# Performance work log

Measured on AMD Instinct MI355X. Metric: run time of the kernel, lower is better.

Reference implementation:

```python
import jax, jax.numpy as jnp
import numpy as np

K1, K2 = 3, 3
DIL = 1
PAD = (DIL * (K1 - 1) // 2, DIL * (K2 - 1) // 2)


def _unfold(x, k1, k2, dilation, padding):
    # x: [B, C, H, W] -> patches [B, C, k1*k2, H*W], matching F.unfold ordering
    B, C, H, W = x.shape
    p0, p1 = padding
    xp = jnp.pad(x, ((0, 0), (0, 0), (p0, p0), (p1, p1)))
    cols = []
    for i in range(k1):  # small fixed loop over kernel taps
        for j in range(k2):
            cols.append(xp[:, :, i * dilation:i * dilation + H, j * dilation:j * dilation + W])
    patches = jnp.stack(cols, axis=2)  # [B, C, k1*k2, H, W]
    return patches.reshape(B, C, k1 * k2, H * W)


def setup_inputs() -> dict:
    key = jax.random.key(0)
    k1, k2, k3, k4 = jax.random.split(key, 4)
    B, Cin, Cout, H, W = 32, 128, 128, 32, 32
    x = jax.random.normal(k1, (B, Cin, H, W), dtype=jnp.float32)
    mask = jax.random.uniform(k2, (1, K1 * K2, H * W), dtype=jnp.float32)
    weight = jax.random.normal(k3, (Cout, Cin, K1, K2), dtype=jnp.float32) * 0.05
    bias = jax.random.normal(k4, (Cout,), dtype=jnp.float32) * 0.05
    return {"x": x, "mask": mask, "weight": weight, "bias": bias}


def reference(x, mask, weight, bias):
    B, Cin, H, W = x.shape
    Cout = weight.shape[0]
    KK = K1 * K2
    # unfold -> [B, Cin, KK, L]
    patches = _unfold(x, K1, K2, DIL, PAD)
    # per-patch mask multiply (mask broadcasts over B and Cin): mask [1, KK, L]
    patches = patches * mask[:, None, :, :]  # [B, Cin, KK, L]
    # dense matmul with flattened weight [Cout, Cin*KK]
    wm = weight.reshape(Cout, Cin * KK)
    out = jnp.einsum('ok,bkl->bol', wm, patches.reshape(B, Cin * KK, H * W))
    out = out + bias[None, :, None]
    return out.reshape(B, Cout, H, W)
```

## Files before the change

kernel.cpp:

```cpp
#include <hip/hip_runtime.h>
#include <hip/hip_fp16.h>

typedef _Float16 half8 __attribute__((ext_vector_type(8)));
typedef float f32x4 __attribute__((ext_vector_type(4)));

#define CIN   128
#define COUT  128
#define HH    32
#define WW    32
#define LTOT  1024
#define KKT   9
#define KDIM  1152

#define ABUF  32768
#define BOFF  65536
#define SMEM_BYTES 114688

__global__ void prep_w_kernel(const float* __restrict__ w, _Float16* __restrict__ wt) {
  int i = blockIdx.x * 256 + threadIdx.x;
  int o = i / KDIM;
  int r = i - o * KDIM;
  int kk = r >> 7, c = r & 127;
  wt[i] = (_Float16)w[(o * CIN + c) * KKT + kk];
}

__device__ __forceinline__ void gld16(const char* g, char* l) {
  __builtin_amdgcn_global_load_lds(
      (const __attribute__((address_space(1))) void*)g,
      (__attribute__((address_space(3))) void*)l, 16, 0, 0);
}

__global__ __launch_bounds__(512, 2)
void conv_mfma_kernel(const float* __restrict__ x,
                      const _Float16* __restrict__ wt,
                      const float* __restrict__ mask,
                      const float* __restrict__ bias,
                      float* __restrict__ out) {
  extern __shared__ char smem[];
  const int tid = threadIdx.x;
  int bid = blockIdx.x;
  bid = (bid & 7) * 32 + (bid >> 3);
  const int b  = bid >> 3;
  const int l0 = (bid & 7) << 7;
  const int h0 = (bid & 7) << 2;

  const int lane = tid & 63, wid = tid >> 6;
  const int lr = lane & 15, lg = lane >> 4;
  const int kh = wid >> 2;
  const int wq = wid & 3;
  const int mw = (wq >> 1) << 6;
  const int nw = (wq & 1) << 6;

  float mv[9][4];
  {
    const float* mr = mask + l0 + nw + lr;
#pragma unroll
    for (int kk = 0; kk < 9; ++kk)
#pragma unroll
      for (int nj = 0; nj < 4; ++nj)
        mv[kk][nj] = mr[kk * LTOT + nj * 16];
  }

  const int wv = tid & 31, q16 = tid >> 5;
  char* bdst = smem + BOFF + wv * 256 + ((q16 ^ (wv & 15)) << 4);
  const float* xb = x + (size_t)b * CIN * LTOT;
  {
    float fr[6][8];
#pragma unroll
    for (int r = 0; r < 6; ++r) {
      const int hg = h0 - 1 + r;
      if ((unsigned)hg < (unsigned)HH) {
        const float* s = xb + (size_t)q16 * 8 * LTOT + hg * WW + wv;
#pragma unroll
        for (int j = 0; j < 8; ++j) fr[r][j] = s[(size_t)j * LTOT];
      }
    }
    asm volatile("s_waitcnt vmcnt(0)" ::: "memory");
#pragma unroll
    for (int r = 0; r < 6; ++r) {
      const int hg = h0 - 1 + r;
      half8 v = (half8){0, 0, 0, 0, 0, 0, 0, 0};
      if ((unsigned)hg < (unsigned)HH) {
#pragma unroll
        for (int j = 0; j < 8; ++j) v[j] = (_Float16)fr[r][j];
      }
      *(half8*)(bdst + r * 8192) = v;
    }
  }
#pragma unroll
  for (int kk = 0; kk < 9; ++kk)
#pragma unroll
    for (int nj = 0; nj < 4; ++nj)
      asm volatile("" : "+v"(mv[kk][nj]));

  const int t4 = tid >> 4, ch = tid & 15;
  const int cx = (ch ^ (t4 & 15)) << 4;
  int asrc[4];
#pragma unroll
  for (int r = 0; r < 4; ++r) asrc[r] = (r * 32 + t4) * 2304 + cx;
  const char* wtc = (const char*)wt;
  auto stageA = [&](int kk) {
    const char* s = wtc + kk * 256;
    char* d = smem + (kk & 1) * ABUF + tid * 16;
#pragma unroll
    for (int r = 0; r < 4; ++r) gld16(s + asrc[r], d + r * 8192);
  };
  stageA(0);
  stageA(1);
  asm volatile("s_waitcnt lgkmcnt(0)" ::: "memory");

  f32x4 acc[4][4];
#pragma unroll
  for (int mi = 0; mi < 4; ++mi)
#pragma unroll
    for (int nj = 0; nj < 4; ++nj)
      acc[mi][nj] = (f32x4){0.f, 0.f, 0.f, 0.f};

#pragma unroll
  for (int kk = 0; kk < 9; ++kk) {
    if (kk < 8) asm volatile("s_waitcnt vmcnt(4)" ::: "memory");
    else        asm volatile("s_waitcnt vmcnt(0)" ::: "memory");
    __builtin_amdgcn_s_barrier();

    const char* A = smem + (kk & 1) * ABUF;
    const int di = (kk * 11) >> 5;
    const int dj = kk - 3 * di;

    const char* Bp[4];
    int xk[4];
    _Float16 mh[4];
#pragma unroll
    for (int nj = 0; nj < 4; ++nj) {
      const int wb = ((nj & 1) << 4) + lr + dj - 1;
      const bool vld = (unsigned)wb < (unsigned)WW;
      const int wc = vld ? wb : 0;
      const int hrow = (nw >> 5) + (nj >> 1) + di;
      Bp[nj] = smem + BOFF + hrow * 8192 + wc * 256;
      xk[nj] = wc & 15;
      mh[nj] = (_Float16)(vld ? mv[kk][nj] : 0.f);
    }
    const char* A0 = A + (mw + lr) * 256;

    __builtin_amdgcn_s_setprio(1);
#pragma unroll
    for (int s = 0; s < 2; ++s) {
      const int q = (kh * 2 + s) * 4 + lg;
      half8 a0 = *(const half8*)(A0 +     0 + ((q ^ lr) << 4));
      half8 a1 = *(const half8*)(A0 +  4096 + ((q ^ lr) << 4));
      half8 a2 = *(const half8*)(A0 +  8192 + ((q ^ lr) << 4));
      half8 a3 = *(const half8*)(A0 + 12288 + ((q ^ lr) << 4));
      half8 b0 = *(const half8*)(Bp[0] + ((q ^ xk[0]) << 4)) * mh[0];
      half8 b1 = *(const half8*)(Bp[1] + ((q ^ xk[1]) << 4)) * mh[1];
      half8 b2 = *(const half8*)(Bp[2] + ((q ^ xk[2]) << 4)) * mh[2];
      half8 b3 = *(const half8*)(Bp[3] + ((q ^ xk[3]) << 4)) * mh[3];
      acc[0][0] = __builtin_amdgcn_mfma_f32_16x16x32_f16(a0, b0, acc[0][0], 0, 0, 0);
      acc[1][0] = __builtin_amdgcn_mfma_f32_16x16x32_f16(a1, b0, acc[1][0], 0, 0, 0);
      acc[2][0] = __builtin_amdgcn_mfma_f32_16x16x32_f16(a2, b0, acc[2][0], 0, 0, 0);
      acc[3][0] = __builtin_amdgcn_mfma_f32_16x16x32_f16(a3, b0, acc[3][0], 0, 0, 0);
      acc[0][1] = __builtin_amdgcn_mfma_f32_16x16x32_f16(a0, b1, acc[0][1], 0, 0, 0);
      acc[1][1] = __builtin_amdgcn_mfma_f32_16x16x32_f16(a1, b1, acc[1][1], 0, 0, 0);
      acc[2][1] = __builtin_amdgcn_mfma_f32_16x16x32_f16(a2, b1, acc[2][1], 0, 0, 0);
      acc[3][1] = __builtin_amdgcn_mfma_f32_16x16x32_f16(a3, b1, acc[3][1], 0, 0, 0);
      acc[0][2] = __builtin_amdgcn_mfma_f32_16x16x32_f16(a0, b2, acc[0][2], 0, 0, 0);
      acc[1][2] = __builtin_amdgcn_mfma_f32_16x16x32_f16(a1, b2, acc[1][2], 0, 0, 0);
      acc[2][2] = __builtin_amdgcn_mfma_f32_16x16x32_f16(a2, b2, acc[2][2], 0, 0, 0);
      acc[3][2] = __builtin_amdgcn_mfma_f32_16x16x32_f16(a3, b2, acc[3][2], 0, 0, 0);
      acc[0][3] = __builtin_amdgcn_mfma_f32_16x16x32_f16(a0, b3, acc[0][3], 0, 0, 0);
      acc[1][3] = __builtin_amdgcn_mfma_f32_16x16x32_f16(a1, b3, acc[1][3], 0, 0, 0);
      acc[2][3] = __builtin_amdgcn_mfma_f32_16x16x32_f16(a2, b3, acc[2][3], 0, 0, 0);
      acc[3][3] = __builtin_amdgcn_mfma_f32_16x16x32_f16(a3, b3, acc[3][3], 0, 0, 0);
    }
    __builtin_amdgcn_s_setprio(0);

    asm volatile("s_waitcnt lgkmcnt(0)" ::: "memory");
    __builtin_amdgcn_s_barrier();
    if (kk <= 6) stageA(kk + 2);
  }

  char* red = smem + wq * 17408 + lane * 272;
  if (kh == 1) {
#pragma unroll
    for (int mi = 0; mi < 4; ++mi)
#pragma unroll
      for (int nj = 0; nj < 4; ++nj)
        *(f32x4*)(red + (mi * 4 + nj) * 16) = acc[mi][nj];
  }
  asm volatile("s_waitcnt lgkmcnt(0)" ::: "memory");
  __builtin_amdgcn_s_barrier();

  if (kh == 0) {
#pragma unroll
    for (int mi = 0; mi < 4; ++mi)
#pragma unroll
      for (int nj = 0; nj < 4; ++nj) {
        f32x4 p = *(const f32x4*)(red + (mi * 4 + nj) * 16);
        acc[mi][nj].x += p.x; acc[mi][nj].y += p.y;
        acc[mi][nj].z += p.z; acc[mi][nj].w += p.w;
      }

    float* outb = out + (size_t)b * COUT * LTOT + l0;
#pragma unroll
    for (int mi = 0; mi < 4; ++mi) {
#pragma unroll
      for (int rr = 0; rr < 4; ++rr) {
        const int o = mw + mi * 16 + lg * 4 + rr;
        const float bv = bias[o];
        float* orow = outb + (size_t)o * LTOT + nw + lr;
#pragma unroll
        for (int nj = 0; nj < 4; ++nj)
          orow[nj * 16] = acc[mi][nj][rr] + bv;
      }
    }
  }
}

extern "C" void kernel_launch(void* const* d_in, const int* in_sizes, int n_in,
                              void* d_out, int out_size, void* d_ws, size_t ws_size,
                              hipStream_t stream) {
  const float* x    = (const float*)d_in[0];
  const float* mask = (const float*)d_in[1];
  const float* w    = (const float*)d_in[2];
  const float* bias = (const float*)d_in[3];
  float* out = (float*)d_out;
  _Float16* wt = (_Float16*)d_ws;

  (void)hipFuncSetAttribute(reinterpret_cast<const void*>(conv_mfma_kernel),
                            hipFuncAttributeMaxDynamicSharedMemorySize, SMEM_BYTES);

  prep_w_kernel<<<576, 256, 0, stream>>>(w, wt);
  conv_mfma_kernel<<<256, 512, SMEM_BYTES, stream>>>(x, wt, mask, bias, out);
}
```

Before: 25.31 us.

## Read weight fragments directly from global memory in MFMA layout, drop LDS staging

The weight prep kernel now writes the fp16 weights pre-permuted into the exact per-lane MFMA fragment order. The conv kernel then loads A operands straight from global memory (L2-resident) instead of double-buffering them through LDS with async loads and per-tap barriers. This removes the per-iteration barriers and the LDS traffic for weights, and shrinks LDS use, which may allow more blocks per CU. In exchange, every wave issues its own global loads with latency exposed inside the MFMA loop, and weight reads are repeated across waves that share the same rows.

```diff
diff --git a/kernel.cpp b/kernel.cpp
--- a/kernel.cpp
+++ b/kernel.cpp
@@ -12,22 +12,16 @@
 #define KKT   9
 #define KDIM  1152
 
-#define ABUF  32768
-#define BOFF  65536
-#define SMEM_BYTES 114688
+#define SMEM_BYTES 69632
 
 __global__ void prep_w_kernel(const float* __restrict__ w, _Float16* __restrict__ wt) {
   int i = blockIdx.x * 256 + threadIdx.x;
-  int o = i / KDIM;
-  int r = i - o * KDIM;
-  int kk = r >> 7, c = r & 127;
+  int q = i >> 10;
+  int o = (i >> 3) & 127;
+  int j = i & 7;
+  int kk = q >> 4;
+  int c  = ((q & 15) << 3) + j;
   wt[i] = (_Float16)w[(o * CIN + c) * KKT + kk];
-}
-
-__device__ __forceinline__ void gld16(const char* g, char* l) {
-  __builtin_amdgcn_global_load_lds(
-      (const __attribute__((address_space(1))) void*)g,
-      (__attribute__((address_space(3))) void*)l, 16, 0, 0);
 }
 
 __global__ __launch_bounds__(512, 2)
@@ -62,7 +56,7 @@
   }
 
   const int wv = tid & 31, q16 = tid >> 5;
-  char* bdst = smem + BOFF + wv * 256 + ((q16 ^ (wv & 15)) << 4);
+  char* bdst = smem + wv * 256 + ((q16 ^ (wv & 15)) << 4);
   const float* xb = x + (size_t)b * CIN * LTOT;
   {
     float fr[6][8];
@@ -92,22 +86,9 @@
 #pragma unroll
     for (int nj = 0; nj < 4; ++nj)
       asm volatile("" : "+v"(mv[kk][nj]));
-
-  const int t4 = tid >> 4, ch = tid & 15;
-  const int cx = (ch ^ (t4 & 15)) << 4;
-  int asrc[4];
-#pragma unroll
-  for (int r = 0; r < 4; ++r) asrc[r] = (r * 32 + t4) * 2304 + cx;
-  const char* wtc = (const char*)wt;
-  auto stageA = [&](int kk) {
-    const char* s = wtc + kk * 256;
-    char* d = smem + (kk & 1) * ABUF + tid * 16;
-#pragma unroll
-    for (int r = 0; r < 4; ++r) gld16(s + asrc[r], d + r * 8192);
-  };
-  stageA(0);
-  stageA(1);
-  asm volatile("s_waitcnt lgkmcnt(0)" ::: "memory");
+  __syncthreads();
+
+  const char* abase = (const char*)wt + lg * 2048 + (mw + lr) * 16;
 
   f32x4 acc[4][4];
 #pragma unroll
@@ -118,11 +99,6 @@
 
 #pragma unroll
   for (int kk = 0; kk < 9; ++kk) {
-    if (kk < 8) asm volatile("s_waitcnt vmcnt(4)" ::: "memory");
-    else        asm volatile("s_waitcnt vmcnt(0)" ::: "memory");
-    __builtin_amdgcn_s_barrier();
-
-    const char* A = smem + (kk & 1) * ABUF;
     const int di = (kk * 11) >> 5;
     const int dj = kk - 3 * di;
 
@@ -135,24 +111,25 @@
       const bool vld = (unsigned)wb < (unsigned)WW;
       const int wc = vld ? wb : 0;
       const int hrow = (nw >> 5) + (nj >> 1) + di;
-      Bp[nj] = smem + BOFF + hrow * 8192 + wc * 256;
+      Bp[nj] = smem + hrow * 8192 + wc * 256;
       xk[nj] = wc & 15;
       mh[nj] = (_Float16)(vld ? mv[kk][nj] : 0.f);
     }
-    const char* A0 = A + (mw + lr) * 256;
 
     __builtin_amdgcn_s_setprio(1);
 #pragma unroll
     for (int s = 0; s < 2; ++s) {
-      const int q = (kh * 2 + s) * 4 + lg;
-      half8 a0 = *(const half8*)(A0 +     0 + ((q ^ lr) << 4));
-      half8 a1 = *(const half8*)(A0 +  4096 + ((q ^ lr) << 4));
-      half8 a2 = *(const half8*)(A0 +  8192 + ((q ^ lr) << 4));
-      half8 a3 = *(const half8*)(A0 + 12288 + ((q ^ lr) << 4));
-      half8 b0 = *(const half8*)(Bp[0] + ((q ^ xk[0]) << 4)) * mh[0];
-      half8 b1 = *(const half8*)(Bp[1] + ((q ^ xk[1]) << 4)) * mh[1];
-      half8 b2 = *(const half8*)(Bp[2] + ((q ^ xk[2]) << 4)) * mh[2];
-      half8 b3 = *(const half8*)(Bp[3] + ((q ^ xk[3]) << 4)) * mh[3];
+      const int qb = kk * 16 + (kh * 2 + s) * 4;
+      const char* ab = abase + qb * 2048;
+      const int q = qb + lg;
+      half8 a0 = *(const half8*)(ab);
+      half8 a1 = *(const half8*)(ab + 256);
+      half8 a2 = *(const half8*)(ab + 512);
+      half8 a3 = *(const half8*)(ab + 768);
+      half8 b0 = *(const half8*)(Bp[0] + (((q & 15) ^ xk[0]) << 4)) * mh[0];
+      half8 b1 = *(const half8*)(Bp[1] + (((q & 15) ^ xk[1]) << 4)) * mh[1];
+      half8 b2 = *(const half8*)(Bp[2] + (((q & 15) ^ xk[2]) << 4)) * mh[2];
+      half8 b3 = *(const half8*)(Bp[3] + (((q & 15) ^ xk[3]) << 4)) * mh[3];
       acc[0][0] = __builtin_amdgcn_mfma_f32_16x16x32_f16(a0, b0, acc[0][0], 0, 0, 0);
       acc[1][0] = __builtin_amdgcn_mfma_f32_16x16x32_f16(a1, b0, acc[1][0], 0, 0, 0);
       acc[2][0] = __builtin_amdgcn_mfma_f32_16x16x32_f16(a2, b0, acc[2][0], 0, 0, 0);
@@ -171,12 +148,9 @@
       acc[3][3] = __builtin_amdgcn_mfma_f32_16x16x32_f16(a3, b3, acc[3][3], 0, 0, 0);
     }
     __builtin_amdgcn_s_setprio(0);
-
-    asm volatile("s_waitcnt lgkmcnt(0)" ::: "memory");
-    __builtin_amdgcn_s_barrier();
-    if (kk <= 6) stageA(kk + 2);
-  }
-
+  }
+
+  __syncthreads();
   char* red = smem + wq * 17408 + lane * 272;
   if (kh == 1) {
 #pragma unroll
@@ -185,8 +159,7 @@
       for (int nj = 0; nj < 4; ++nj)
         *(f32x4*)(red + (mi * 4 + nj) * 16) = acc[mi][nj];
   }
-  asm volatile("s_waitcnt lgkmcnt(0)" ::: "memory");
-  __builtin_amdgcn_s_barrier();
+  __syncthreads();
 
   if (kh == 0) {
 #pragma unroll
```

New measurement: 26.06 us, median of 2. 3.0% more time.
